# Performance work log

Measured on AMD Instinct MI355X. Metric: run time of the kernel, lower is better.

## Reference

```python
import jax, jax.numpy as jnp
import numpy as np

N_NODES = 50000


def setup_inputs() -> dict:
    key = jax.random.key(0)
    ks = jax.random.split(key, 5)
    d_in, d_out = 512, 512
    n_edges = 800000
    x = jax.random.normal(ks[0], (N_NODES, d_in), dtype=jnp.float32)
    edge_index = jax.random.randint(ks[1], (2, n_edges), 0, N_NODES, dtype=jnp.int64)
    s = 1.0 / np.sqrt(d_in)
    W_l = jax.random.uniform(ks[2], (d_out, d_in), dtype=jnp.float32, minval=-s, maxval=s)
    b_l = jax.random.uniform(ks[3], (d_out,), dtype=jnp.float32, minval=-s, maxval=s)
    W_r = jax.random.uniform(ks[4], (d_out, d_in), dtype=jnp.float32, minval=-s, maxval=s)
    return {"x": x, "edge_index": edge_index, "W_l": W_l, "b_l": b_l, "W_r": W_r}


def reference(x, edge_index, W_l, b_l, W_r):
    # lin_l: dense transform before aggregation
    x_l = x @ W_l.T + b_l                       # [N, d_out]
    src, dst = edge_index[0], edge_index[1]
    # sparse adjacency matmul (SAGE mean-neighbor aggregation):
    # out_l[i] = mean_{j in N(i)} x_l[j]
    agg = jax.ops.segment_sum(x_l[src], dst, num_segments=N_NODES)   # [N, d_out]
    deg = jax.ops.segment_sum(jnp.ones_like(src, dtype=x.dtype), dst,
                              num_segments=N_NODES)                  # [N]
    out_l = agg / jnp.maximum(deg, 1.0)[:, None]
    # lin_r: self-loop transform (no bias)
    out_r = x @ W_r.T
    return out_l + out_r
```

## Files before the change

### kernel.cpp

```cpp
#include <hip/hip_runtime.h>

typedef __bf16 bf16x8 __attribute__((ext_vector_type(8)));
typedef float floatx4 __attribute__((ext_vector_type(4)));
typedef float floatx2 __attribute__((ext_vector_type(2)));
typedef unsigned short ushortx8 __attribute__((ext_vector_type(8)));

__device__ __forceinline__ unsigned short f2b(float f) {
    union { float f; unsigned u; } v; v.f = f;
    unsigned r = v.u + 0x7fffu + ((v.u >> 16) & 1u);
    return (unsigned short)(r >> 16);
}


__global__ void scan1_kernel(const int* __restrict__ deg, int* __restrict__ bsum, int n) {
    __shared__ int s[256];
    int b = blockIdx.x, t = threadIdx.x;
    int base = b * 1024 + t * 4;
    int v = 0;
#pragma unroll
    for (int i = 0; i < 4; i++) { int idx = base + i; if (idx < n) v += deg[idx]; }
    s[t] = v; __syncthreads();
    for (int o = 128; o > 0; o >>= 1) { if (t < o) s[t] += s[t + o]; __syncthreads(); }
    if (t == 0) bsum[b] = s[0];
}

__global__ void scan3_kernel(const int* __restrict__ deg, const int* __restrict__ bsum,
                             int* __restrict__ off, int n, int nb, int nE) {
    __shared__ int s[256];
    __shared__ int base_s;
    int b = blockIdx.x, t = threadIdx.x;
    if (t < 64) {
        int v = (t < nb && t < b) ? bsum[t] : 0;
        for (int o = 32; o > 0; o >>= 1) v += __shfl_down(v, o, 64);
        if (t == 0) base_s = v;
    }
    int idx = b * 1024 + t * 4;
    int a0 = (idx     < n) ? deg[idx]     : 0;
    int a1 = (idx + 1 < n) ? deg[idx + 1] : 0;
    int a2 = (idx + 2 < n) ? deg[idx + 2] : 0;
    int a3 = (idx + 3 < n) ? deg[idx + 3] : 0;
    int tsum = a0 + a1 + a2 + a3;
    s[t] = tsum; __syncthreads();
    for (int o = 1; o < 256; o <<= 1) {
        int u = (t >= o) ? s[t - o] : 0;
        __syncthreads();
        s[t] += u;
        __syncthreads();
    }
    int excl = s[t] - tsum + base_s;
    if (idx     < n) off[idx]     = excl;
    if (idx + 1 < n) off[idx + 1] = excl + a0;
    if (idx + 2 < n) off[idx + 2] = excl + a0 + a1;
    if (idx + 3 < n) off[idx + 3] = excl + a0 + a1 + a2;
    if (b == 0 && t == 0) off[n] = nE;
}

__global__ void fill_kernel(const int* __restrict__ src, const int* __restrict__ dst,
                            const int* __restrict__ off, int* __restrict__ cursor,
                            int* __restrict__ csr, int nE) {
    int e = blockIdx.x * blockDim.x + threadIdx.x;
    if (e < nE) {
        int d = dst[e];
        int pos = atomicAdd(&cursor[d], 1);
        csr[off[d] + pos] = src[e];
    }
}


__global__ void conv_kernel(const float* __restrict__ x, unsigned short* __restrict__ Abuf,
                            unsigned char* __restrict__ X8,
                            const float* __restrict__ Wl, const float* __restrict__ Wr,
                            unsigned short* __restrict__ Wcat,
                            const int* __restrict__ dst, int* __restrict__ deg, int nE,
                            int Mreal, long nx) {
    long t = (long)blockIdx.x * blockDim.x + threadIdx.x;
    if (t < nx) {
        long row = t >> 6;
        int c8 = (int)(t & 63) * 8;
        if (row < Mreal) {
            const float4* p4 = (const float4*)(x + row * 512 + c8);
            float4 v0 = p4[0], v1 = p4[1];
            ushortx8 o8;
            o8[0] = f2b(v0.x); o8[1] = f2b(v0.y); o8[2] = f2b(v0.z); o8[3] = f2b(v0.w);
            o8[4] = f2b(v1.x); o8[5] = f2b(v1.y); o8[6] = f2b(v1.z); o8[7] = f2b(v1.w);
            *(ushortx8*)(Abuf + row * 1024 + 512 + c8) = o8;
            unsigned int pa = __builtin_amdgcn_cvt_pk_fp8_f32(v0.x, v0.y, 0, false);
            pa = __builtin_amdgcn_cvt_pk_fp8_f32(v0.z, v0.w, pa, true);
            unsigned int pb = __builtin_amdgcn_cvt_pk_fp8_f32(v1.x, v1.y, 0, false);
            pb = __builtin_amdgcn_cvt_pk_fp8_f32(v1.z, v1.w, pb, true);
            *(uint2*)(X8 + row * 512 + c8) = make_uint2(pa, pb);
        } else {
            ushortx8 z = {0, 0, 0, 0, 0, 0, 0, 0};
            *(ushortx8*)(Abuf + row * 1024 + c8) = z;
            *(ushortx8*)(Abuf + row * 1024 + 512 + c8) = z;
        }
    } else {
        long u = t - nx;
        if (u < 65536) {
            int o = (int)(u >> 7);
            int c8 = (int)(u & 127) * 8;
            const float* p = (c8 < 512) ? (Wl + o * 512 + c8) : (Wr + o * 512 + (c8 - 512));
            float4 v0 = ((const float4*)p)[0], v1 = ((const float4*)p)[1];
            ushortx8 o8;
            o8[0] = f2b(v0.x); o8[1] = f2b(v0.y); o8[2] = f2b(v0.z); o8[3] = f2b(v0.w);
            o8[4] = f2b(v1.x); o8[5] = f2b(v1.y); o8[6] = f2b(v1.z); o8[7] = f2b(v1.w);
            *(ushortx8*)(Wcat + (long)o * 1024 + c8) = o8;
        } else {
            long v = u - 65536;
            if (v < nE) atomicAdd(&deg[dst[v]], 1);
        }
    }
}


__device__ __forceinline__ uint2 ldrow(const unsigned char* __restrict__ X8, int myi, int idx, int l) {
    int s = __builtin_amdgcn_readlane(myi, idx);
    return *(const uint2*)(X8 + (long)s * 512 + l * 8);
}

__device__ __forceinline__ void accum(float* a, uint2 p) {
    floatx2 f0 = __builtin_amdgcn_cvt_pk_f32_fp8(p.x, false);
    floatx2 f1 = __builtin_amdgcn_cvt_pk_f32_fp8(p.x, true);
    floatx2 f2 = __builtin_amdgcn_cvt_pk_f32_fp8(p.y, false);
    floatx2 f3 = __builtin_amdgcn_cvt_pk_f32_fp8(p.y, true);
    a[0] += f0[0]; a[1] += f0[1]; a[2] += f1[0]; a[3] += f1[1];
    a[4] += f2[0]; a[5] += f2[1]; a[6] += f3[0]; a[7] += f3[1];
}

__global__ void agg_kernel(const unsigned char* __restrict__ X8,
                           const int* __restrict__ off, const int* __restrict__ csr,
                           unsigned short* __restrict__ Abuf_w, int n) {
    int wid = (int)((blockIdx.x * (long)blockDim.x + threadIdx.x) >> 6);
    int l = threadIdx.x & 63;
    if (wid >= n) return;
    int beg = off[wid], end = off[wid + 1];
    float a[8] = {};
    int e = beg;
    while (e < end) {
        int cnt = end - e; if (cnt > 64) cnt = 64;
        int myi = csr[e + (l < cnt ? l : cnt - 1)];
        int c1 = cnt - 1;
        uint2 b0 = ldrow(X8, myi, 0, l);
        uint2 b1 = ldrow(X8, myi, 1 < c1 ? 1 : c1, l);
        uint2 b2 = ldrow(X8, myi, 2 < c1 ? 2 : c1, l);
        uint2 b3 = ldrow(X8, myi, 3 < c1 ? 3 : c1, l);
        int j = 0;
        for (; j + 4 < cnt; j += 4) {
            uint2 n0 = ldrow(X8, myi, j + 4, l);
            uint2 n1 = ldrow(X8, myi, j + 5 < c1 ? j + 5 : c1, l);
            uint2 n2 = ldrow(X8, myi, j + 6 < c1 ? j + 6 : c1, l);
            uint2 n3 = ldrow(X8, myi, j + 7 < c1 ? j + 7 : c1, l);
            accum(a, b0); accum(a, b1); accum(a, b2); accum(a, b3);
            b0 = n0; b1 = n1; b2 = n2; b3 = n3;
        }
        int rem = cnt - j;
        accum(a, b0);
        if (rem > 1) accum(a, b1);
        if (rem > 2) accum(a, b2);
        if (rem > 3) accum(a, b3);
        e += cnt;
    }
    int d = end - beg;
    float inv = 1.0f / (float)(d > 0 ? d : 1);
    ushortx8 o8;
#pragma unroll
    for (int i = 0; i < 8; i++) o8[i] = f2b(a[i] * inv);
    *(ushortx8*)(Abuf_w + (long)wid * 1024 + l * 8) = o8;
}


__global__ __launch_bounds__(256, 3)
void gemm_kernel(const unsigned short* __restrict__ A, const unsigned short* __restrict__ B,
                 const float* __restrict__ bl, const int* __restrict__ deg,
                 float* __restrict__ out, int Mreal, int nby) {
    int L = blockIdx.x;
    int by = (L >> 5) * 8 + (L & 7);
    int bx = (L >> 3) & 3;
    if (by >= nby) return;

    __shared__ unsigned short As[3 * 128 * 32];
    __shared__ unsigned short Bs[3 * 128 * 32];
    int tid = threadIdx.x;
    int w = tid >> 6, l = tid & 63;
    long i0 = (long)by * 128;
    int n0 = bx * 128;
    int wm = (w >> 1) * 64, wn = (w & 1) * 64;
    int r = l & 15, q = l >> 4;
    int srow = l >> 2;
    int cg8 = ((l & 3) ^ ((srow >> 1) & 3)) * 8;
    int p8 = (q ^ ((r >> 1) & 3)) * 8;

    floatx4 acc[4][4] = {};

    auto stage = [&](int buf, int k0) {
#pragma unroll
        for (int j = 0; j < 2; j++) {
            int s = w * 2 + j;
            int row = s * 16 + srow;
            const unsigned short* ga = A + (i0 + row) * 1024 + k0 + cg8;
            const unsigned short* gb = B + (long)(n0 + row) * 1024 + k0 + cg8;
            __builtin_amdgcn_global_load_lds(
                (__attribute__((address_space(1))) void*)(uintptr_t)ga,
                (__attribute__((address_space(3))) void*)(uintptr_t)(As + buf * 4096 + s * 512), 16, 0, 0);
            __builtin_amdgcn_global_load_lds(
                (__attribute__((address_space(1))) void*)(uintptr_t)gb,
                (__attribute__((address_space(3))) void*)(uintptr_t)(Bs + buf * 4096 + s * 512), 16, 0, 0);
        }
    };

    auto compute = [&](int cur) {
        bf16x8 af[4], bfr[4];
        const unsigned short* Ab = As + cur * 4096;
        const unsigned short* Bb = Bs + cur * 4096;
#pragma unroll
        for (int a = 0; a < 4; a++)
            af[a] = *(const bf16x8*)(Ab + (wm + a * 16 + r) * 32 + p8);
#pragma unroll
        for (int b = 0; b < 4; b++)
            bfr[b] = *(const bf16x8*)(Bb + (wn + b * 16 + r) * 32 + p8);
        __builtin_amdgcn_s_setprio(1);
#pragma unroll
        for (int a = 0; a < 4; a++)
#pragma unroll
            for (int b = 0; b < 4; b++)
                acc[a][b] = __builtin_amdgcn_mfma_f32_16x16x32_bf16(bfr[b], af[a], acc[a][b], 0, 0, 0);
        __builtin_amdgcn_s_setprio(0);
    };

    stage(0, 0);
    stage(1, 32);
    int cur = 0;
    for (int t = 0; t < 31; ++t) {
        asm volatile("s_waitcnt vmcnt(4)" ::: "memory");
        __builtin_amdgcn_sched_barrier(0);
        __builtin_amdgcn_s_barrier();
        __builtin_amdgcn_sched_barrier(0);
        if (t + 2 < 32) {
            int nb2 = cur + 2; if (nb2 >= 3) nb2 -= 3;
            stage(nb2, (t + 2) * 32);
        }
        compute(cur);
        cur++; if (cur >= 3) cur -= 3;
    }
    asm volatile("s_waitcnt vmcnt(0)" ::: "memory");
    __builtin_amdgcn_sched_barrier(0);
    __builtin_amdgcn_s_barrier();
    __builtin_amdgcn_sched_barrier(0);
    compute(cur);

#pragma unroll
    for (int a = 0; a < 4; a++) {
        long row = i0 + wm + a * 16 + r;
        if (row < Mreal) {
            bool hasdeg = deg[row] > 0;
#pragma unroll
            for (int b = 0; b < 4; b++) {
                int col0 = n0 + wn + b * 16 + q * 4;
                floatx4 v = acc[a][b];
                if (hasdeg) {
                    float4 bb = *(const float4*)(bl + col0);
                    v[0] += bb.x; v[1] += bb.y; v[2] += bb.z; v[3] += bb.w;
                }
                *(floatx4*)(out + row * 512 + col0) = v;
            }
        }
    }
}


extern "C" void kernel_launch(void* const* d_in, const int* in_sizes, int n_in,
                              void* d_out, int out_size, void* d_ws, size_t ws_size,
                              hipStream_t stream) {
    const float* x  = (const float*)d_in[0];
    const int* eidx = (const int*)d_in[1];
    const float* Wl = (const float*)d_in[2];
    const float* bl = (const float*)d_in[3];
    const float* Wr = (const float*)d_in[4];
    float* out = (float*)d_out;

    int N  = in_sizes[0] / 512;
    int nE = in_sizes[1] / 2;
    const int* src = eidx;
    const int* dst = eidx + nE;
    int Mpad = (N + 127) & ~127;
    int nb = (N + 1023) / 1024;
    int nby = Mpad / 128;

    char* w = (char*)d_ws;
    size_t o = 0;
    auto alloc = [&](size_t bytes) { void* p = w + o; o = (o + bytes + 255) & ~255UL; return p; };
    int* deg    = (int*)alloc((size_t)N * 4);
    int* cursor = (int*)alloc((size_t)N * 4);
    int* off    = (int*)alloc((size_t)(N + 1) * 4);
    int* bsum   = (int*)alloc((size_t)nb * 4);
    int* csr    = (int*)alloc((size_t)nE * 4);
    unsigned short* Wcat = (unsigned short*)alloc((size_t)512 * 1024 * 2);
    unsigned short* Abuf = (unsigned short*)alloc((size_t)Mpad * 1024 * 2);
    unsigned char*  X8   = (unsigned char*)alloc((size_t)Mpad * 512);
    if (o > ws_size) return;

    hipMemsetAsync(deg, 0, (size_t)N * 4, stream);
    hipMemsetAsync(cursor, 0, (size_t)N * 4, stream);

    long nx = (long)Mpad * 64;
    long ntot = nx + 65536 + nE;
    conv_kernel<<<(int)((ntot + 255) / 256), 256, 0, stream>>>(x, Abuf, X8, Wl, Wr, Wcat,
                                                               dst, deg, nE, N, nx);
    scan1_kernel<<<nb, 256, 0, stream>>>(deg, bsum, N);
    scan3_kernel<<<nb, 256, 0, stream>>>(deg, bsum, off, N, nb, nE);
    fill_kernel<<<(nE + 255) / 256, 256, 0, stream>>>(src, dst, off, cursor, csr, nE);
    agg_kernel<<<(N * 64 + 255) / 256, 256, 0, stream>>>(X8, off, csr, Abuf, N);

    int nbyp = (nby + 7) & ~7;
    gemm_kernel<<<nbyp * 4, 256, 0, stream>>>(Abuf, Wcat, bl, deg, out, N, nby);
}
```

Measured before the change: 393.8 us.

## Load GEMM B operand directly from global into registers, bypassing LDS

The weight (B) tiles are no longer staged through shared memory. Each wave now loads its B fragments straight from global memory into registers, double-buffered one k-step ahead, and the main loop is unrolled by two to alternate the register buffers. This halves LDS footprint and LDS read traffic, which may let more blocks fit per CU. In exchange, each wave issues its own uncoalesced 16-byte global loads, and B rows are re-fetched by every wave that shares them. Register pressure also rises.

```diff
diff --git a/kernel.cpp b/kernel.cpp
--- a/kernel.cpp
+++ b/kernel.cpp
@@ -179,7 +179,6 @@
     if (by >= nby) return;
 
     __shared__ unsigned short As[3 * 128 * 32];
-    __shared__ unsigned short Bs[3 * 128 * 32];
     int tid = threadIdx.x;
     int w = tid >> 6, l = tid & 63;
     long i0 = (long)by * 128;
@@ -191,6 +190,7 @@
     int p8 = (q ^ ((r >> 1) & 3)) * 8;
 
     floatx4 acc[4][4] = {};
+    bf16x8 Ba[4], Bb[4];
 
     auto stage = [&](int buf, int k0) {
 #pragma unroll
@@ -198,55 +198,69 @@
             int s = w * 2 + j;
             int row = s * 16 + srow;
             const unsigned short* ga = A + (i0 + row) * 1024 + k0 + cg8;
-            const unsigned short* gb = B + (long)(n0 + row) * 1024 + k0 + cg8;
             __builtin_amdgcn_global_load_lds(
                 (__attribute__((address_space(1))) void*)(uintptr_t)ga,
                 (__attribute__((address_space(3))) void*)(uintptr_t)(As + buf * 4096 + s * 512), 16, 0, 0);
-            __builtin_amdgcn_global_load_lds(
-                (__attribute__((address_space(1))) void*)(uintptr_t)gb,
-                (__attribute__((address_space(3))) void*)(uintptr_t)(Bs + buf * 4096 + s * 512), 16, 0, 0);
         }
     };
 
-    auto compute = [&](int cur) {
-        bf16x8 af[4], bfr[4];
-        const unsigned short* Ab = As + cur * 4096;
-        const unsigned short* Bb = Bs + cur * 4096;
+    auto loadB = [&](bf16x8 (&Bf)[4], int k0) {
+#pragma unroll
+        for (int b = 0; b < 4; b++)
+            Bf[b] = *(const bf16x8*)(B + (long)(n0 + wn + b * 16 + r) * 1024 + k0 + q * 8);
+    };
+
+    auto compute = [&](int bu, bf16x8 (&Bf)[4]) {
+        const unsigned short* Ab = As + bu * 4096;
+        bf16x8 af[4];
 #pragma unroll
         for (int a = 0; a < 4; a++)
             af[a] = *(const bf16x8*)(Ab + (wm + a * 16 + r) * 32 + p8);
-#pragma unroll
-        for (int b = 0; b < 4; b++)
-            bfr[b] = *(const bf16x8*)(Bb + (wn + b * 16 + r) * 32 + p8);
         __builtin_amdgcn_s_setprio(1);
 #pragma unroll
         for (int a = 0; a < 4; a++)
 #pragma unroll
             for (int b = 0; b < 4; b++)
-                acc[a][b] = __builtin_amdgcn_mfma_f32_16x16x32_bf16(bfr[b], af[a], acc[a][b], 0, 0, 0);
+                acc[a][b] = __builtin_amdgcn_mfma_f32_16x16x32_bf16(Bf[b], af[a], acc[a][b], 0, 0, 0);
         __builtin_amdgcn_s_setprio(0);
     };
 
     stage(0, 0);
+    loadB(Ba, 0);
     stage(1, 32);
-    int cur = 0;
-    for (int t = 0; t < 31; ++t) {
-        asm volatile("s_waitcnt vmcnt(4)" ::: "memory");
+
+    for (int t = 0; t < 30; t += 2) {
+        asm volatile("s_waitcnt vmcnt(2)" ::: "memory");
         __builtin_amdgcn_sched_barrier(0);
         __builtin_amdgcn_s_barrier();
         __builtin_amdgcn_sched_barrier(0);
-        if (t + 2 < 32) {
-            int nb2 = cur + 2; if (nb2 >= 3) nb2 -= 3;
-            stage(nb2, (t + 2) * 32);
-        }
-        compute(cur);
-        cur++; if (cur >= 3) cur -= 3;
-    }
+        loadB(Bb, (t + 1) * 32);
+        __builtin_amdgcn_sched_barrier(0);
+        stage((t + 2) % 3, (t + 2) * 32);
+        __builtin_amdgcn_sched_barrier(0);
+        compute(t % 3, Ba);
+        asm volatile("s_waitcnt vmcnt(2)" ::: "memory");
+        __builtin_amdgcn_sched_barrier(0);
+        __builtin_amdgcn_s_barrier();
+        __builtin_amdgcn_sched_barrier(0);
+        loadB(Ba, (t + 2) * 32);
+        __builtin_amdgcn_sched_barrier(0);
+        stage((t + 3) % 3, (t + 3) * 32);
+        __builtin_amdgcn_sched_barrier(0);
+        compute((t + 1) % 3, Bb);
+    }
+    asm volatile("s_waitcnt vmcnt(2)" ::: "memory");
+    __builtin_amdgcn_sched_barrier(0);
+    __builtin_amdgcn_s_barrier();
+    __builtin_amdgcn_sched_barrier(0);
+    loadB(Bb, 31 * 32);
+    __builtin_amdgcn_sched_barrier(0);
+    compute(0, Ba);
     asm volatile("s_waitcnt vmcnt(0)" ::: "memory");
     __builtin_amdgcn_sched_barrier(0);
     __builtin_amdgcn_s_barrier();
     __builtin_amdgcn_sched_barrier(0);
-    compute(cur);
+    compute(1, Bb);
 
 #pragma unroll
     for (int a = 0; a < 4; a++) {
```

Measured after the change: 449.2 us. 1.14x slower.
